# Kernel optimization log

Measured on AMD Instinct MI355X. Metric: run time of the kernel, lower is better.

Reference implementation:

```python
import jax, jax.numpy as jnp
import numpy as np

N, E, G = 50000, 800000, 512
HD, ED, GD, HID = 128, 64, 64, 128  # h_dim, e_dim, g_dim, hid_dim


def _mlp2(x, W1, b1, W2, b2, last_act):
    # Linear -> ReLU -> Linear (-> optional last activation)
    y = jax.nn.relu(x @ W1 + b1) @ W2 + b2
    return last_act(y) if last_act is not None else y


def setup_inputs() -> dict:
    key = jax.random.key(0)
    ks = list(jax.random.split(key, 24))
    ki = iter(ks)

    def p(shape):
        return (jax.random.normal(next(ki), shape, jnp.float32) * 0.02)

    inp = {
        "h": jax.random.normal(next(ki), (N, HD), jnp.float32),
        "e_index": jax.random.randint(next(ki), (2, E), 0, N),
        "e": jax.random.normal(next(ki), (E, ED), jnp.float32),
        "g": jax.random.normal(next(ki), (G, GD), jnp.float32),
        "batch": jnp.sort(jax.random.randint(next(ki), (N,), 0, G)),
        # fc_m: [2*HD+ED+GD, HID, HID], last_activation=relu
        "W_m1": p((2 * HD + ED + GD, HID)), "b_m1": jnp.zeros((HID,), jnp.float32),
        "W_m2": p((HID, HID)), "b_m2": jnp.zeros((HID,), jnp.float32),
        # fc_m_att: [HID, 1], sigmoid
        "W_ma": p((HID, 1)), "b_ma": jnp.zeros((1,), jnp.float32),
        # fc_e: [HID, ED, ED]
        "W_e1": p((HID, ED)), "b_e1": jnp.zeros((ED,), jnp.float32),
        "W_e2": p((ED, ED)), "b_e2": jnp.zeros((ED,), jnp.float32),
        # fc_h: [HD+HID+GD, HD, HD]
        "W_h1": p((HD + HID + GD, HD)), "b_h1": jnp.zeros((HD,), jnp.float32),
        "W_h2": p((HD, HD)), "b_h2": jnp.zeros((HD,), jnp.float32),
        # fc_h_att: [HD, 1]
        "W_ha": p((HD, 1)), "b_ha": jnp.zeros((1,), jnp.float32),
        # fc_g: [GD+HD, GD, GD]
        "W_g1": p((GD + HD, GD)), "b_g1": jnp.zeros((GD,), jnp.float32),
        "W_g2": p((GD, GD)), "b_g2": jnp.zeros((GD,), jnp.float32),
    }
    return inp


def reference(h, e_index, e, g, batch,
              W_m1, b_m1, W_m2, b_m2, W_ma, b_ma,
              W_e1, b_e1, W_e2, b_e2,
              W_h1, b_h1, W_h2, b_h2, W_ha, b_ha,
              W_g1, b_g1, W_g2, b_g2):
    src, dst = e_index[0], e_index[1]
    e_batch = batch[dst]

    # edge message: concat gathered endpoints + edge feat + gathered global
    m_cat = jnp.concatenate([h[src], h[dst], e, g[e_batch]], axis=1)  # [E, 2HD+ED+GD]
    m = jax.nn.relu(jax.nn.relu(m_cat @ W_m1 + b_m1) @ W_m2 + b_m2)   # [E, HID]
    m_att = jax.nn.sigmoid(m @ W_ma + b_ma)                            # [E, 1]

    e_update = _mlp2(m, W_e1, b_e1, W_e2, b_e2, None)                  # [E, ED]
    e_out = jax.nn.relu(e + e_update)

    m_aggr = jax.ops.segment_sum(m_att * m, dst, num_segments=h.shape[0])  # [N, HID]

    h_cat = jnp.concatenate([h, m_aggr, g[batch]], axis=1)             # [N, HD+HID+GD]
    h_update = _mlp2(h_cat, W_h1, b_h1, W_h2, b_h2, None)
    h_out = jax.nn.relu(h + h_update)                                  # [N, HD]
    h_att = h_out @ W_ha + b_ha                                        # [N, 1]

    h_aggr = jax.ops.segment_sum(h_att * h_out, batch, num_segments=g.shape[0])  # [G, HD]

    g_cat = jnp.concatenate([g, h_aggr], axis=1)                       # [G, GD+HD]
    g_update = _mlp2(g_cat, W_g1, b_g1, W_g2, b_g2, None)
    g_out = jax.nn.relu(g + g_update)

    return (h_out, e_out, g_out)
```

## Files before the change

kernel.cpp:

```cpp
#include <hip/hip_runtime.h>
#include <hip/hip_bf16.h>

#define NN 50000
#define NE 800000
#define NG 512
#define HD 128
#define ED 64
#define GD 64
#define HID 128
#define EB 64

typedef __attribute__((ext_vector_type(8))) short short8;
typedef __attribute__((ext_vector_type(4))) short short4v;
typedef __attribute__((ext_vector_type(2))) float f32x2;
typedef __attribute__((ext_vector_type(4))) float f32x4;

__device__ __forceinline__ short f2bf(float f) {
  union { float f; unsigned u; } v; v.f = f;
  unsigned r = v.u + 0x7fffu + ((v.u >> 16) & 1u);
  return (short)(r >> 16);
}

__device__ __forceinline__ float bf2f(short s) {
  union { unsigned u; float f; } v;
  v.u = ((unsigned)(unsigned short)s) << 16;
  return v.f;
}

__device__ __forceinline__ short8 load_a8(const float* p) {
  const f32x4* q = (const f32x4*)p;
  f32x4 x0 = q[0], x1 = q[1];
  short8 r;
  r[0]=f2bf(x0[0]); r[1]=f2bf(x0[1]); r[2]=f2bf(x0[2]); r[3]=f2bf(x0[3]);
  r[4]=f2bf(x1[0]); r[5]=f2bf(x1[1]); r[6]=f2bf(x1[2]); r[7]=f2bf(x1[3]);
  return r;
}

__device__ __forceinline__ int swz(int row, int col, int rowBytes) {
  int b = row * rowBytes + col * 2;
  b ^= (row & 7) << 4;
  return b >> 1;
}

__global__ void pack_kernel(const float* __restrict__ Wm1, const float* __restrict__ Wm2,
                            const float* __restrict__ We1, const float* __restrict__ We2,
                            const float* __restrict__ Wh1, const float* __restrict__ Wh2,
                            short* __restrict__ out) {
  int gid = blockIdx.x * 256 + threadIdx.x;
  if (gid >= 135168) return;
  const float* W; int Ncol, base, idx;
  if (gid < 49152)       { W = Wm1; Ncol = 128; base = 0;      idx = gid; }
  else if (gid < 65536)  { W = Wm2; Ncol = 128; base = 49152;  idx = gid - 49152; }
  else if (gid < 73728)  { W = We1; Ncol = 64;  base = 65536;  idx = gid - 65536; }
  else if (gid < 77824)  { W = We2; Ncol = 64;  base = 73728;  idx = gid - 73728; }
  else if (gid < 118784) { W = Wh1; Ncol = 128; base = 77824;  idx = gid - 77824; }
  else                   { W = Wh2; Ncol = 128; base = 118784; idx = gid - 118784; }
  int k = idx / Ncol, n = idx % Ncol;
  out[base + (k >> 3) * Ncol * 8 + n * 8 + (k & 7)] = f2bf(W[idx]);
}

__global__ void cast_kernel(const float* __restrict__ h, const float* __restrict__ g,
                            const float* __restrict__ e, const int* __restrict__ ei,
                            short* __restrict__ h_bf, short* __restrict__ g_bf,
                            short* __restrict__ e_bf, int* __restrict__ deg) {
  int gid = blockIdx.x * 256 + threadIdx.x;
  const int H4 = NN * HD / 4;
  const int G4 = NG * GD / 4;
  const int E4 = NE * ED / 4;
  if (gid < H4) {
    f32x4 v = ((const f32x4*)h)[gid];
    short4v r; r[0]=f2bf(v[0]); r[1]=f2bf(v[1]); r[2]=f2bf(v[2]); r[3]=f2bf(v[3]);
    *(short4v*)(h_bf + gid * 4) = r;
  } else if (gid < H4 + G4) {
    int i = gid - H4;
    f32x4 v = ((const f32x4*)g)[i];
    short4v r; r[0]=f2bf(v[0]); r[1]=f2bf(v[1]); r[2]=f2bf(v[2]); r[3]=f2bf(v[3]);
    *(short4v*)(g_bf + i * 4) = r;
  } else if (gid < H4 + G4 + E4) {
    int i = gid - H4 - G4;
    f32x4 v = ((const f32x4*)e)[i];
    short4v r; r[0]=f2bf(v[0]); r[1]=f2bf(v[1]); r[2]=f2bf(v[2]); r[3]=f2bf(v[3]);
    *(short4v*)(e_bf + i * 4) = r;
  } else if (gid < H4 + G4 + E4 + NE) {
    int i = gid - H4 - G4 - E4;
    atomicAdd(&deg[ei[NE + i]], 1);
  }
}

__global__ __launch_bounds__(1024) void scan_kernel(int* __restrict__ deg) {
  __shared__ int psum[1024];
  const int CH = 49;
  int t = threadIdx.x;
  int lo = t * CH, hi = lo + CH; if (hi > NN) hi = NN; if (lo > NN) lo = NN;
  int s = 0;
  for (int i = lo; i < hi; ++i) s += deg[i];
  psum[t] = s;
  __syncthreads();
  for (int d = 1; d < 1024; d <<= 1) {
    int v = (t >= d) ? psum[t - d] : 0;
    __syncthreads();
    psum[t] += v;
    __syncthreads();
  }
  int run = (t == 0) ? 0 : psum[t - 1];
  for (int i = lo; i < hi; ++i) { int v = deg[i]; deg[i] = run; run += v; }
}

__global__ void scatter_kernel(const int* __restrict__ ei, int* __restrict__ off,
                               int* __restrict__ elist) {
  int i = blockIdx.x * 256 + threadIdx.x;
  if (i < NE) {
    int d = ei[NE + i];
    int p = atomicAdd(&off[d], 1);
    elist[p] = i;
  }
}

__global__ __launch_bounds__(256) void edge_kernel(
    const short* __restrict__ h_bf, const int* __restrict__ ei,
    const short* __restrict__ e_bf, const short* __restrict__ g_bf,
    const int* __restrict__ batch, const int* __restrict__ elist,
    const short* __restrict__ pWm1, const float* __restrict__ bm1,
    const short* __restrict__ pWm2, const float* __restrict__ bm2,
    const float* __restrict__ Wma, const float* __restrict__ bma,
    const short* __restrict__ pWe1, const float* __restrict__ be1,
    const short* __restrict__ pWe2, const float* __restrict__ be2,
    float* __restrict__ e_out, float* __restrict__ m_aggr) {
  __shared__ short lds_m[EB * 128];
  __shared__ float att_s[EB];
  __shared__ int sdst[EB];
  __shared__ int seid[EB];
  short* ebuf = lds_m;

  const int tid = threadIdx.x;
  const int w = tid >> 6;
  const int lane = tid & 63;
  const int row16 = lane & 15;
  const int quad = lane >> 4;
  const int eb = blockIdx.x * EB;

  if (tid < EB) {
    int eid = elist[eb + tid];
    seid[tid] = eid;
    sdst[tid] = ei[NE + eid];
  }

  const int eidr = elist[eb + w * 16 + row16];
  const int dstr = ei[NE + eidr];
  const int srcr = ei[eidr];
  const int gbr = batch[dstr];

  const short* seg0 = h_bf + (size_t)srcr * HD;
  const short* seg1 = h_bf + (size_t)dstr * HD;
  const short* seg2 = e_bf + (size_t)eidr * ED;
  const short* seg3 = g_bf + (size_t)gbr * GD;

  f32x4 acc[8];
#pragma unroll
  for (int t = 0; t < 8; ++t) acc[t] = (f32x4)0.0f;
#pragma unroll
  for (int c = 0; c < 12; ++c) {
    const short* src; int off;
    if (c < 4)       { src = seg0; off = c * 32; }
    else if (c < 8)  { src = seg1; off = (c - 4) * 32; }
    else if (c < 10) { src = seg2; off = (c - 8) * 32; }
    else             { src = seg3; off = (c - 10) * 32; }
    short8 a = *(const short8*)(src + off + quad * 8);
    const short* bp = pWm1 + (size_t)(c * 4 + quad) * (HID * 8) + row16 * 8;
#pragma unroll
    for (int t = 0; t < 8; ++t) {
      short8 b = *(const short8*)(bp + t * 16 * 8);
      acc[t] = __builtin_amdgcn_mfma_f32_16x16x32_bf16(a, b, acc[t], 0, 0, 0);
    }
  }
#pragma unroll
  for (int t = 0; t < 8; ++t) {
    float b1 = bm1[t * 16 + row16];
#pragma unroll
    for (int r = 0; r < 4; ++r) {
      float y = fmaxf(acc[t][r] + b1, 0.f);
      lds_m[swz(w * 16 + quad * 4 + r, t * 16 + row16, 256)] = f2bf(y);
    }
  }

  f32x4 acc2[8];
#pragma unroll
  for (int t = 0; t < 8; ++t) acc2[t] = (f32x4)0.0f;
#pragma unroll
  for (int c = 0; c < 4; ++c) {
    short8 a = *(const short8*)&lds_m[swz(w * 16 + row16, c * 32 + quad * 8, 256)];
    const short* bp = pWm2 + (size_t)(c * 4 + quad) * (HID * 8) + row16 * 8;
#pragma unroll
    for (int t = 0; t < 8; ++t) {
      short8 b = *(const short8*)(bp + t * 16 * 8);
      acc2[t] = __builtin_amdgcn_mfma_f32_16x16x32_bf16(a, b, acc2[t], 0, 0, 0);
    }
  }

  float p[4] = {0.f, 0.f, 0.f, 0.f};
#pragma unroll
  for (int t = 0; t < 8; ++t) {
    float b2 = bm2[t * 16 + row16];
    float wv = Wma[t * 16 + row16];
#pragma unroll
    for (int r = 0; r < 4; ++r) {
      float y = fmaxf(acc2[t][r] + b2, 0.f);
      lds_m[swz(w * 16 + quad * 4 + r, t * 16 + row16, 256)] = f2bf(y);
      p[r] += y * wv;
    }
  }

#pragma unroll
  for (int s = 1; s < 16; s <<= 1) {
#pragma unroll
    for (int r = 0; r < 4; ++r) p[r] += __shfl_xor(p[r], s, 64);
  }
  {
    float bma0 = bma[0];
    if (row16 == 0) {
#pragma unroll
      for (int r = 0; r < 4; ++r)
        att_s[w * 16 + quad * 4 + r] = 1.f / (1.f + __expf(-(p[r] + bma0)));
    }
  }

  f32x4 acc3[4];
#pragma unroll
  for (int t = 0; t < 4; ++t) acc3[t] = (f32x4)0.0f;
#pragma unroll
  for (int c = 0; c < 4; ++c) {
    short8 a = *(const short8*)&lds_m[swz(w * 16 + row16, c * 32 + quad * 8, 256)];
    const short* bp = pWe1 + (size_t)(c * 4 + quad) * (ED * 8) + row16 * 8;
#pragma unroll
    for (int t = 0; t < 4; ++t) {
      short8 b = *(const short8*)(bp + t * 16 * 8);
      acc3[t] = __builtin_amdgcn_mfma_f32_16x16x32_bf16(a, b, acc3[t], 0, 0, 0);
    }
  }

  __syncthreads();

  {
    int cp = tid & 63;
    int r0 = (tid >> 6) * 16;
    int cur = sdst[r0];
    float s0 = 0.f, s1 = 0.f;
    bool first = true;
#pragma unroll 1
    for (int r = r0; r < r0 + 16; ++r) {
      int d = sdst[r];
      unsigned u = *(const unsigned*)&lds_m[swz(r, cp * 2, 256)];
      float av = att_s[r];
      float v0 = bf2f((short)(u & 0xffffu)) * av;
      float v1 = bf2f((short)(u >> 16)) * av;
      if (d != cur) {
        if (first) {
          atomicAdd(&m_aggr[(size_t)cur * HID + cp * 2], s0);
          atomicAdd(&m_aggr[(size_t)cur * HID + cp * 2 + 1], s1);
        } else {
          f32x2 st; st[0] = s0; st[1] = s1;
          *(f32x2*)&m_aggr[(size_t)cur * HID + cp * 2] = st;
        }
        first = false; cur = d; s0 = v0; s1 = v1;
      } else {
        s0 += v0; s1 += v1;
      }
    }
    atomicAdd(&m_aggr[(size_t)cur * HID + cp * 2], s0);
    atomicAdd(&m_aggr[(size_t)cur * HID + cp * 2 + 1], s1);
  }

  __syncthreads();

#pragma unroll
  for (int t = 0; t < 4; ++t) {
    float b1 = be1[t * 16 + row16];
#pragma unroll
    for (int r = 0; r < 4; ++r) {
      float y = fmaxf(acc3[t][r] + b1, 0.f);
      ebuf[swz(w * 16 + quad * 4 + r, t * 16 + row16, 128)] = f2bf(y);
    }
  }

  f32x4 acc4[4];
#pragma unroll
  for (int t = 0; t < 4; ++t) acc4[t] = (f32x4)0.0f;
#pragma unroll
  for (int c = 0; c < 2; ++c) {
    short8 a = *(const short8*)&ebuf[swz(w * 16 + row16, c * 32 + quad * 8, 128)];
    const short* bp = pWe2 + (size_t)(c * 4 + quad) * (ED * 8) + row16 * 8;
#pragma unroll
    for (int t = 0; t < 4; ++t) {
      short8 b = *(const short8*)(bp + t * 16 * 8);
      acc4[t] = __builtin_amdgcn_mfma_f32_16x16x32_bf16(a, b, acc4[t], 0, 0, 0);
    }
  }

  int eidS[4];
#pragma unroll
  for (int r = 0; r < 4; ++r) eidS[r] = seid[w * 16 + quad * 4 + r];
#pragma unroll
  for (int t = 0; t < 4; ++t) {
    float b2 = be2[t * 16 + row16];
#pragma unroll
    for (int r = 0; r < 4; ++r) {
      int col = t * 16 + row16;
      float res = bf2f(e_bf[(size_t)eidS[r] * ED + col]);
      float v = res + acc4[t][r] + b2;
      e_out[(size_t)eidS[r] * ED + col] = fmaxf(v, 0.f);
    }
  }
}

__global__ __launch_bounds__(256) void node_kernel(
    const float* __restrict__ h, const short* __restrict__ h_bf,
    const float* __restrict__ m_aggr, const short* __restrict__ g_bf,
    const int* __restrict__ batch,
    const short* __restrict__ pWh1, const float* __restrict__ bh1,
    const short* __restrict__ pWh2, const float* __restrict__ bh2,
    const float* __restrict__ Wha, const float* __restrict__ bha,
    float* __restrict__ h_out, float* __restrict__ h_aggr) {
  __shared__ short lds_y[4][16 * 128];
  __shared__ int sbat[64];

  const int wave = threadIdx.x >> 6;
  const int lane = threadIdx.x & 63;
  const int row16 = lane & 15;
  const int quad = lane >> 4;
  const int nbase = blockIdx.x * 64 + wave * 16;

  int nA = nbase + row16;
  int nAc = nA < NN ? nA : NN - 1;
  int gbA = batch[nAc];
  if (quad == 0) sbat[wave * 16 + row16] = (nA < NN) ? gbA : -1;

  short8 afr[10];
  {
    const short* s0 = h_bf + (size_t)nAc * HD;
    const float* s1 = m_aggr + (size_t)nAc * HID;
    const short* s2 = g_bf + (size_t)gbA * GD;
#pragma unroll
    for (int c = 0; c < 4; ++c) afr[c] = *(const short8*)(s0 + c * 32 + quad * 8);
#pragma unroll
    for (int c = 0; c < 4; ++c) afr[4 + c] = load_a8(s1 + c * 32 + quad * 8);
    afr[8] = *(const short8*)(s2 + quad * 8);
    afr[9] = *(const short8*)(s2 + 32 + quad * 8);
  }

  f32x4 acc[8];
#pragma unroll
  for (int t = 0; t < 8; ++t) acc[t] = (f32x4)0.0f;
#pragma unroll
  for (int c = 0; c < 10; ++c) {
    const short* bp = pWh1 + (size_t)(c * 4 + quad) * HD * 8 + row16 * 8;
#pragma unroll
    for (int t = 0; t < 8; ++t) {
      short8 b = *(const short8*)(bp + t * 16 * 8);
      acc[t] = __builtin_amdgcn_mfma_f32_16x16x32_bf16(afr[c], b, acc[t], 0, 0, 0);
    }
  }
#pragma unroll
  for (int t = 0; t < 8; ++t) {
    float b1 = bh1[t * 16 + row16];
#pragma unroll
    for (int r = 0; r < 4; ++r) {
      float y = fmaxf(acc[t][r] + b1, 0.f);
      lds_y[wave][swz(quad * 4 + r, t * 16 + row16, 256)] = f2bf(y);
    }
  }

  f32x4 acc2[8];
#pragma unroll
  for (int t = 0; t < 8; ++t) acc2[t] = (f32x4)0.0f;
#pragma unroll
  for (int c = 0; c < 4; ++c) {
    short8 a = *(const short8*)&lds_y[wave][swz(row16, c * 32 + quad * 8, 256)];
    const short* bp = pWh2 + (size_t)(c * 4 + quad) * HD * 8 + row16 * 8;
#pragma unroll
    for (int t = 0; t < 8; ++t) {
      short8 b = *(const short8*)(bp + t * 16 * 8);
      acc2[t] = __builtin_amdgcn_mfma_f32_16x16x32_bf16(a, b, acc2[t], 0, 0, 0);
    }
  }

  float hval[8][4];
  int nS[4];
#pragma unroll
  for (int r = 0; r < 4; ++r) nS[r] = nbase + quad * 4 + r;
#pragma unroll
  for (int t = 0; t < 8; ++t) {
    float b2 = bh2[t * 16 + row16];
#pragma unroll
    for (int r = 0; r < 4; ++r) {
      float v = 0.f;
      if (nS[r] < NN) {
        v = h[(size_t)nS[r] * HD + t * 16 + row16] + acc2[t][r] + b2;
        v = fmaxf(v, 0.f);
        h_out[(size_t)nS[r] * HD + t * 16 + row16] = v;
      }
      hval[t][r] = v;
    }
  }

  float part[4] = {0.f, 0.f, 0.f, 0.f};
#pragma unroll
  for (int t = 0; t < 8; ++t) {
    float w = Wha[t * 16 + row16];
#pragma unroll
    for (int r = 0; r < 4; ++r) part[r] += hval[t][r] * w;
  }
#pragma unroll
  for (int s = 1; s < 16; s <<= 1) {
#pragma unroll
    for (int r = 0; r < 4; ++r) part[r] += __shfl_xor(part[r], s, 64);
  }
  float bha0 = bha[0];
#pragma unroll
  for (int t = 0; t < 8; ++t)
#pragma unroll
    for (int r = 0; r < 4; ++r)
      lds_y[wave][swz(quad * 4 + r, t * 16 + row16, 256)] =
          f2bf((part[r] + bha0) * hval[t][r]);

  __syncthreads();

  {
    int col = threadIdx.x & 127;
    int r0 = (threadIdx.x >> 7) * 32;
    int cur = sbat[r0];
    float sum = 0.f;
    bool first = true;
#pragma unroll 1
    for (int r = r0; r < r0 + 32; ++r) {
      int d = sbat[r];
      float v = bf2f(lds_y[r >> 4][swz(r & 15, col, 256)]);
      if (d != cur) {
        if (cur >= 0) {
          if (first) atomicAdd(&h_aggr[(size_t)cur * HD + col], sum);
          else h_aggr[(size_t)cur * HD + col] = sum;
        }
        first = false; cur = d; sum = v;
      } else {
        sum += v;
      }
    }
    if (cur >= 0) atomicAdd(&h_aggr[(size_t)cur * HD + col], sum);
  }
}

__global__ void g_kernel(const float* __restrict__ g, const float* __restrict__ h_aggr,
                         const float* __restrict__ Wg1, const float* __restrict__ bg1,
                         const float* __restrict__ Wg2, const float* __restrict__ bg2,
                         float* __restrict__ g_out) {
  __shared__ float cat[192];
  __shared__ float y1[64];
  int r = blockIdx.x;
  int t = threadIdx.x;
  cat[t] = g[(size_t)r * GD + t];
  cat[64 + t] = h_aggr[(size_t)r * HD + t];
  cat[128 + t] = h_aggr[(size_t)r * HD + 64 + t];
  __syncthreads();
  float a = bg1[t];
  for (int k = 0; k < 192; ++k) a += cat[k] * Wg1[k * 64 + t];
  y1[t] = fmaxf(a, 0.f);
  __syncthreads();
  float b = bg2[t];
  for (int k = 0; k < 64; ++k) b += y1[k] * Wg2[k * 64 + t];
  float v = g[(size_t)r * GD + t] + b;
  g_out[(size_t)r * GD + t] = fmaxf(v, 0.f);
}

extern "C" void kernel_launch(void* const* d_in, const int* in_sizes, int n_in,
                              void* d_out, int out_size, void* d_ws, size_t ws_size,
                              hipStream_t stream) {
  const float* h = (const float*)d_in[0];
  const int* ei = (const int*)d_in[1];
  const float* e = (const float*)d_in[2];
  const float* g = (const float*)d_in[3];
  const int* batch = (const int*)d_in[4];
  const float* Wm1 = (const float*)d_in[5];
  const float* bm1 = (const float*)d_in[6];
  const float* Wm2 = (const float*)d_in[7];
  const float* bm2 = (const float*)d_in[8];
  const float* Wma = (const float*)d_in[9];
  const float* bma = (const float*)d_in[10];
  const float* We1 = (const float*)d_in[11];
  const float* be1 = (const float*)d_in[12];
  const float* We2 = (const float*)d_in[13];
  const float* be2 = (const float*)d_in[14];
  const float* Wh1 = (const float*)d_in[15];
  const float* bh1 = (const float*)d_in[16];
  const float* Wh2 = (const float*)d_in[17];
  const float* bh2 = (const float*)d_in[18];
  const float* Wha = (const float*)d_in[19];
  const float* bha = (const float*)d_in[20];
  const float* Wg1 = (const float*)d_in[21];
  const float* bg1 = (const float*)d_in[22];
  const float* Wg2 = (const float*)d_in[23];
  const float* bg2 = (const float*)d_in[24];

  float* out = (float*)d_out;
  float* h_out = out;
  float* e_out = out + (size_t)NN * HD;
  float* g_out = e_out + (size_t)NE * ED;

  char* ws = (char*)d_ws;
  float* m_aggr = (float*)ws;
  float* h_aggr = (float*)(ws + 25600000);
  short* packed = (short*)(ws + 25862144);
  int* deg      = (int*)(ws + 26132480);
  int* elist    = (int*)(ws + 26332480);
  short* h_bf   = (short*)(ws + 29532480);
  short* g_bf   = (short*)(ws + 42332480);
  short* e_bf   = (short*)(ws + 42398016);
  short* pWm1 = packed;
  short* pWm2 = packed + 49152;
  short* pWe1 = packed + 65536;
  short* pWe2 = packed + 73728;
  short* pWh1 = packed + 77824;
  short* pWh2 = packed + 118784;

  hipMemsetAsync(m_aggr, 0, (size_t)NN * HID * 4, stream);
  hipMemsetAsync(h_aggr, 0, (size_t)NG * HD * 4, stream);
  hipMemsetAsync(deg, 0, (size_t)NN * 4, stream);

  pack_kernel<<<(135168 + 255) / 256, 256, 0, stream>>>(Wm1, Wm2, We1, We2, Wh1, Wh2, packed);
  cast_kernel<<<(15208192 + 255) / 256, 256, 0, stream>>>(h, g, e, ei, h_bf, g_bf, e_bf, deg);
  scan_kernel<<<1, 1024, 0, stream>>>(deg);
  scatter_kernel<<<(NE + 255) / 256, 256, 0, stream>>>(ei, deg, elist);

  edge_kernel<<<NE / EB, 256, 0, stream>>>(h_bf, ei, e_bf, g_bf, batch, elist,
                                           pWm1, bm1, pWm2, bm2, Wma, bma,
                                           pWe1, be1, pWe2, be2, e_out, m_aggr);

  node_kernel<<<(NN + 63) / 64, 256, 0, stream>>>(h, h_bf, m_aggr, g_bf, batch,
                                                  pWh1, bh1, pWh2, bh2, Wha, bha,
                                                  h_out, h_aggr);

  g_kernel<<<NG, 64, 0, stream>>>(g, h_aggr, Wg1, bg1, Wg2, bg2, g_out);
}
```

Before: 690.0 us.

## Double edge tile per block and stage MLP weights in LDS with double buffering

The edge block grows to 128 edges, so each wave now computes two 16-row M tiles. Each B fragment is reused for two MFMAs, halving weight-fragment reads per edge. The first two message-MLP weight matrices are staged chunk by chunk into a double-buffered LDS area with block syncs, instead of being read per wave from global memory. In exchange, accumulator registers and LDS use roughly double, which may lower occupancy, and the staging loop adds per-chunk barriers.

```diff
diff --git a/kernel.cpp b/kernel.cpp
--- a/kernel.cpp
+++ b/kernel.cpp
@@ -8,7 +8,7 @@
 #define ED 64
 #define GD 64
 #define HID 128
-#define EB 64
+#define EB 128
 
 typedef __attribute__((ext_vector_type(8))) short short8;
 typedef __attribute__((ext_vector_type(4))) short short4v;
@@ -127,6 +127,7 @@
     const short* __restrict__ pWe2, const float* __restrict__ be2,
     float* __restrict__ e_out, float* __restrict__ m_aggr) {
   __shared__ short lds_m[EB * 128];
+  __shared__ short bufB[2][4096];
   __shared__ float att_s[EB];
   __shared__ int sdst[EB];
   __shared__ int seid[EB];
@@ -139,102 +140,141 @@
   const int quad = lane >> 4;
   const int eb = blockIdx.x * EB;
 
+#define STAGE(Wp, c, b) do {                                              \
+    short8 v0 = *(const short8*)((Wp) + (size_t)(c) * 4096 + tid * 8);    \
+    short8 v1 = *(const short8*)((Wp) + (size_t)(c) * 4096 + 2048 + tid * 8); \
+    *(short8*)&bufB[(b)][tid * 8] = v0;                                   \
+    *(short8*)&bufB[(b)][2048 + tid * 8] = v1;                            \
+  } while (0)
+
   if (tid < EB) {
     int eid = elist[eb + tid];
     seid[tid] = eid;
     sdst[tid] = ei[NE + eid];
   }
 
-  const int eidr = elist[eb + w * 16 + row16];
-  const int dstr = ei[NE + eidr];
-  const int srcr = ei[eidr];
-  const int gbr = batch[dstr];
-
-  const short* seg0 = h_bf + (size_t)srcr * HD;
-  const short* seg1 = h_bf + (size_t)dstr * HD;
-  const short* seg2 = e_bf + (size_t)eidr * ED;
-  const short* seg3 = g_bf + (size_t)gbr * GD;
-
-  f32x4 acc[8];
-#pragma unroll
-  for (int t = 0; t < 8; ++t) acc[t] = (f32x4)0.0f;
+  const short* pa[2][4];
+#pragma unroll
+  for (int m = 0; m < 2; ++m) {
+    int eid = elist[eb + w * 32 + m * 16 + row16];
+    int dst = ei[NE + eid];
+    int src = ei[eid];
+    int gb = batch[dst];
+    pa[m][0] = h_bf + (size_t)src * HD + quad * 8;
+    pa[m][1] = h_bf + (size_t)dst * HD + quad * 8;
+    pa[m][2] = e_bf + (size_t)eid * ED + quad * 8;
+    pa[m][3] = g_bf + (size_t)gb * GD + quad * 8;
+  }
+
+  f32x4 acc[2][8];
+#pragma unroll
+  for (int m = 0; m < 2; ++m)
+#pragma unroll
+    for (int t = 0; t < 8; ++t) acc[m][t] = (f32x4)0.0f;
+
+  STAGE(pWm1, 0, 0);
+  __syncthreads();
 #pragma unroll
   for (int c = 0; c < 12; ++c) {
-    const short* src; int off;
-    if (c < 4)       { src = seg0; off = c * 32; }
-    else if (c < 8)  { src = seg1; off = (c - 4) * 32; }
-    else if (c < 10) { src = seg2; off = (c - 8) * 32; }
-    else             { src = seg3; off = (c - 10) * 32; }
-    short8 a = *(const short8*)(src + off + quad * 8);
-    const short* bp = pWm1 + (size_t)(c * 4 + quad) * (HID * 8) + row16 * 8;
+    if (c + 1 < 12) STAGE(pWm1, c + 1, (c + 1) & 1);
+    const int seg = (c < 4) ? 0 : (c < 8) ? 1 : (c < 10) ? 2 : 3;
+    const int off = ((c < 4) ? c : (c < 8) ? c - 4 : (c < 10) ? c - 8 : c - 10) * 32;
+    short8 a0 = *(const short8*)(pa[0][seg] + off);
+    short8 a1 = *(const short8*)(pa[1][seg] + off);
+    const short* bc = &bufB[c & 1][0];
 #pragma unroll
     for (int t = 0; t < 8; ++t) {
-      short8 b = *(const short8*)(bp + t * 16 * 8);
-      acc[t] = __builtin_amdgcn_mfma_f32_16x16x32_bf16(a, b, acc[t], 0, 0, 0);
-    }
-  }
-#pragma unroll
-  for (int t = 0; t < 8; ++t) {
-    float b1 = bm1[t * 16 + row16];
-#pragma unroll
-    for (int r = 0; r < 4; ++r) {
-      float y = fmaxf(acc[t][r] + b1, 0.f);
-      lds_m[swz(w * 16 + quad * 4 + r, t * 16 + row16, 256)] = f2bf(y);
-    }
-  }
-
-  f32x4 acc2[8];
-#pragma unroll
-  for (int t = 0; t < 8; ++t) acc2[t] = (f32x4)0.0f;
+      short8 b = *(const short8*)(bc + quad * 1024 + (t * 16 + row16) * 8);
+      acc[0][t] = __builtin_amdgcn_mfma_f32_16x16x32_bf16(a0, b, acc[0][t], 0, 0, 0);
+      acc[1][t] = __builtin_amdgcn_mfma_f32_16x16x32_bf16(a1, b, acc[1][t], 0, 0, 0);
+    }
+    __syncthreads();
+  }
+
+#pragma unroll
+  for (int m = 0; m < 2; ++m)
+#pragma unroll
+    for (int t = 0; t < 8; ++t) {
+      float b1 = bm1[t * 16 + row16];
+#pragma unroll
+      for (int r = 0; r < 4; ++r) {
+        float y = fmaxf(acc[m][t][r] + b1, 0.f);
+        lds_m[swz(w * 32 + m * 16 + quad * 4 + r, t * 16 + row16, 256)] = f2bf(y);
+      }
+    }
+
+  f32x4 acc2[2][8];
+#pragma unroll
+  for (int m = 0; m < 2; ++m)
+#pragma unroll
+    for (int t = 0; t < 8; ++t) acc2[m][t] = (f32x4)0.0f;
+
+  STAGE(pWm2, 0, 0);
+  __syncthreads();
 #pragma unroll
   for (int c = 0; c < 4; ++c) {
-    short8 a = *(const short8*)&lds_m[swz(w * 16 + row16, c * 32 + quad * 8, 256)];
-    const short* bp = pWm2 + (size_t)(c * 4 + quad) * (HID * 8) + row16 * 8;
+    if (c + 1 < 4) STAGE(pWm2, c + 1, (c + 1) & 1);
+    short8 a0 = *(const short8*)&lds_m[swz(w * 32 + row16, c * 32 + quad * 8, 256)];
+    short8 a1 = *(const short8*)&lds_m[swz(w * 32 + 16 + row16, c * 32 + quad * 8, 256)];
+    const short* bc = &bufB[c & 1][0];
 #pragma unroll
     for (int t = 0; t < 8; ++t) {
-      short8 b = *(const short8*)(bp + t * 16 * 8);
-      acc2[t] = __builtin_amdgcn_mfma_f32_16x16x32_bf16(a, b, acc2[t], 0, 0, 0);
-    }
-  }
-
-  float p[4] = {0.f, 0.f, 0.f, 0.f};
-#pragma unroll
-  for (int t = 0; t < 8; ++t) {
-    float b2 = bm2[t * 16 + row16];
-    float wv = Wma[t * 16 + row16];
-#pragma unroll
-    for (int r = 0; r < 4; ++r) {
-      float y = fmaxf(acc2[t][r] + b2, 0.f);
-      lds_m[swz(w * 16 + quad * 4 + r, t * 16 + row16, 256)] = f2bf(y);
-      p[r] += y * wv;
-    }
-  }
+      short8 b = *(const short8*)(bc + quad * 1024 + (t * 16 + row16) * 8);
+      acc2[0][t] = __builtin_amdgcn_mfma_f32_16x16x32_bf16(a0, b, acc2[0][t], 0, 0, 0);
+      acc2[1][t] = __builtin_amdgcn_mfma_f32_16x16x32_bf16(a1, b, acc2[1][t], 0, 0, 0);
+    }
+    __syncthreads();
+  }
+
+  float p[2][4] = {{0.f, 0.f, 0.f, 0.f}, {0.f, 0.f, 0.f, 0.f}};
+#pragma unroll
+  for (int m = 0; m < 2; ++m)
+#pragma unroll
+    for (int t = 0; t < 8; ++t) {
+      float b2 = bm2[t * 16 + row16];
+      float wv = Wma[t * 16 + row16];
+#pragma unroll
+      for (int r = 0; r < 4; ++r) {
+        float y = fmaxf(acc2[m][t][r] + b2, 0.f);
+        lds_m[swz(w * 32 + m * 16 + quad * 4 + r, t * 16 + row16, 256)] = f2bf(y);
+        p[m][r] += y * wv;
+      }
+    }
 
 #pragma unroll
   for (int s = 1; s < 16; s <<= 1) {
 #pragma unroll
-    for (int r = 0; r < 4; ++r) p[r] += __shfl_xor(p[r], s, 64);
+    for (int m = 0; m < 2; ++m)
+#pragma unroll
+      for (int r = 0; r < 4; ++r) p[m][r] += __shfl_xor(p[m][r], s, 64);
   }
   {
     float bma0 = bma[0];
     if (row16 == 0) {
 #pragma unroll
-      for (int r = 0; r < 4; ++r)
-        att_s[w * 16 + quad * 4 + r] = 1.f / (1.f + __expf(-(p[r] + bma0)));
-    }
-  }
-
-  f32x4 acc3[4];
-#pragma unroll
-  for (int t = 0; t < 4; ++t) acc3[t] = (f32x4)0.0f;
+      for (int m = 0; m < 2; ++m)
+#pragma unroll
+        for (int r = 0; r < 4; ++r)
+          att_s[w * 32 + m * 16 + quad * 4 + r] =
+              1.f / (1.f + __expf(-(p[m][r] + bma0)));
+    }
+  }
+
+  f32x4 acc3[2][4];
+#pragma unroll
+  for (int m = 0; m < 2; ++m)
+#pragma unroll
+    for (int t = 0; t < 4; ++t) acc3[m][t] = (f32x4)0.0f;
 #pragma unroll
   for (int c = 0; c < 4; ++c) {
-    short8 a = *(const short8*)&lds_m[swz(w * 16 + row16, c * 32 + quad * 8, 256)];
+    short8 a0 = *(const short8*)&lds_m[swz(w * 32 + row16, c * 32 + quad * 8, 256)];
+    short8 a1 = *(const short8*)&lds_m[swz(w * 32 + 16 + row16, c * 32 + quad * 8, 256)];
     const short* bp = pWe1 + (size_t)(c * 4 + quad) * (ED * 8) + row16 * 8;
 #pragma unroll
     for (int t = 0; t < 4; ++t) {
       short8 b = *(const short8*)(bp + t * 16 * 8);
-      acc3[t] = __builtin_amdgcn_mfma_f32_16x16x32_bf16(a, b, acc3[t], 0, 0, 0);
+      acc3[0][t] = __builtin_amdgcn_mfma_f32_16x16x32_bf16(a0, b, acc3[0][t], 0, 0, 0);
+      acc3[1][t] = __builtin_amdgcn_mfma_f32_16x16x32_bf16(a1, b, acc3[1][t], 0, 0, 0);
     }
   }
 
@@ -242,12 +282,12 @@
 
   {
     int cp = tid & 63;
-    int r0 = (tid >> 6) * 16;
+    int r0 = (tid >> 6) * 32;
     int cur = sdst[r0];
     float s0 = 0.f, s1 = 0.f;
     bool first = true;
 #pragma unroll 1
-    for (int r = r0; r < r0 + 16; ++r) {
+    for (int r = r0; r < r0 + 32; ++r) {
       int d = sdst[r];
       unsigned u = *(const unsigned*)&lds_m[swz(r, cp * 2, 256)];
       float av = att_s[r];
@@ -273,43 +313,51 @@
   __syncthreads();
 
 #pragma unroll
-  for (int t = 0; t < 4; ++t) {
-    float b1 = be1[t * 16 + row16];
-#pragma unroll
-    for (int r = 0; r < 4; ++r) {
-      float y = fmaxf(acc3[t][r] + b1, 0.f);
-      ebuf[swz(w * 16 + quad * 4 + r, t * 16 + row16, 128)] = f2bf(y);
-    }
-  }
-
-  f32x4 acc4[4];
-#pragma unroll
-  for (int t = 0; t < 4; ++t) acc4[t] = (f32x4)0.0f;
+  for (int m = 0; m < 2; ++m)
+#pragma unroll
+    for (int t = 0; t < 4; ++t) {
+      float b1 = be1[t * 16 + row16];
+#pragma unroll
+      for (int r = 0; r < 4; ++r) {
+        float y = fmaxf(acc3[m][t][r] + b1, 0.f);
+        ebuf[swz(w * 32 + m * 16 + quad * 4 + r, t * 16 + row16, 128)] = f2bf(y);
+      }
+    }
+
+  f32x4 acc4[2][4];
+#pragma unroll
+  for (int m = 0; m < 2; ++m)
+#pragma unroll
+    for (int t = 0; t < 4; ++t) acc4[m][t] = (f32x4)0.0f;
 #pragma unroll
   for (int c = 0; c < 2; ++c) {
-    short8 a = *(const short8*)&ebuf[swz(w * 16 + row16, c * 32 + quad * 8, 128)];
+    short8 a0 = *(const short8*)&ebuf[swz(w * 32 + row16, c * 32 + quad * 8, 128)];
+    short8 a1 = *(const short8*)&ebuf[swz(w * 32 + 16 + row16, c * 32 + quad * 8, 128)];
     const short* bp = pWe2 + (size_t)(c * 4 + quad) * (ED * 8) + row16 * 8;
 #pragma unroll
     for (int t = 0; t < 4; ++t) {
       short8 b = *(const short8*)(bp + t * 16 * 8);
-      acc4[t] = __builtin_amdgcn_mfma_f32_16x16x32_bf16(a, b, acc4[t], 0, 0, 0);
-    }
-  }
-
-  int eidS[4];
-#pragma unroll
-  for (int r = 0; r < 4; ++r) eidS[r] = seid[w * 16 + quad * 4 + r];
-#pragma unroll
-  for (int t = 0; t < 4; ++t) {
-    float b2 = be2[t * 16 + row16];
-#pragma unroll
-    for (int r = 0; r < 4; ++r) {
-      int col = t * 16 + row16;
-      float res = bf2f(e_bf[(size_t)eidS[r] * ED + col]);
-      float v = res + acc4[t][r] + b2;
-      e_out[(size_t)eidS[r] * ED + col] = fmaxf(v, 0.f);
-    }
-  }
+      acc4[0][t] = __builtin_amdgcn_mfma_f32_16x16x32_bf16(a0, b, acc4[0][t], 0, 0, 0);
+      acc4[1][t] = __builtin_amdgcn_mfma_f32_16x16x32_bf16(a1, b, acc4[1][t], 0, 0, 0);
+    }
+  }
+
+#pragma unroll
+  for (int m = 0; m < 2; ++m)
+#pragma unroll
+    for (int t = 0; t < 4; ++t) {
+      float b2 = be2[t * 16 + row16];
+#pragma unroll
+      for (int r = 0; r < 4; ++r) {
+        int row = w * 32 + m * 16 + quad * 4 + r;
+        int eid = seid[row];
+        int col = t * 16 + row16;
+        float res = bf2f(e_bf[(size_t)eid * ED + col]);
+        float v = res + acc4[m][t][r] + b2;
+        e_out[(size_t)eid * ED + col] = fmaxf(v, 0.f);
+      }
+    }
+#undef STAGE
 }
 
 __global__ __launch_bounds__(256) void node_kernel(
```

Measured after the change: 849.9 us. +23.2%, slower.
